# Kernel optimization log

Hardware: AMD Instinct MI355X
Metric: run time of the kernel (lower is better)

The kernel has to match this reference:

```python
import jax, jax.numpy as jnp
import numpy as np

D_MODEL = 2048
N_HEADS = 32
N_KV_HEADS = 8
HEAD_DIM = D_MODEL // N_HEADS  # 64
N_REP = N_HEADS // N_KV_HEADS  # 4
SCALE = HEAD_DIM ** -0.5


def _rope_tables(seq_len):
    inv_freq = 1.0 / (10000.0 ** (jnp.arange(0, HEAD_DIM, 2, dtype=jnp.float32) / HEAD_DIM))
    t = jnp.arange(seq_len, dtype=jnp.float32)
    freqs = jnp.outer(t, inv_freq)  # [S, HEAD_DIM/2]
    return jnp.cos(freqs), jnp.sin(freqs)


def _apply_rope(x, cos, sin):
    # x: [b, h, s, d]; interleaved even/odd rotation, matching torch stack+flatten
    x_r, x_i = x[..., ::2], x[..., 1::2]
    out_r = x_r * cos - x_i * sin
    out_i = x_r * sin + x_i * cos
    out = jnp.stack([out_r, out_i], axis=-1)  # [b,h,s,d/2,2]
    return out.reshape(x.shape)


def setup_inputs() -> dict:
    key = jax.random.key(0)
    ks = jax.random.split(key, 5)
    bs, seq_len = 2, 2048
    std = D_MODEL ** -0.5
    x = jax.random.normal(ks[0], (bs, seq_len, D_MODEL), dtype=jnp.float32)
    wq = jax.random.normal(ks[1], (N_HEADS * HEAD_DIM, D_MODEL), dtype=jnp.float32) * std
    wk = jax.random.normal(ks[2], (N_KV_HEADS * HEAD_DIM, D_MODEL), dtype=jnp.float32) * std
    wv = jax.random.normal(ks[3], (N_KV_HEADS * HEAD_DIM, D_MODEL), dtype=jnp.float32) * std
    wo = jax.random.normal(ks[4], (D_MODEL, N_HEADS * HEAD_DIM), dtype=jnp.float32) * std
    return {"x": x, "wq": wq, "wk": wk, "wv": wv, "wo": wo}


def reference(x, wq, wk, wv, wo):
    bs, seq_len, _ = x.shape
    # fused-style QKV projections (nn.Linear: x @ W.T)
    q = (x @ wq.T).reshape(bs, seq_len, N_HEADS, HEAD_DIM).transpose(0, 2, 1, 3)
    k = (x @ wk.T).reshape(bs, seq_len, N_KV_HEADS, HEAD_DIM).transpose(0, 2, 1, 3)
    v = (x @ wv.T).reshape(bs, seq_len, N_KV_HEADS, HEAD_DIM).transpose(0, 2, 1, 3)
    cos, sin = _rope_tables(seq_len)  # [S, HEAD_DIM/2], broadcast over b,h
    q = _apply_rope(q, cos, sin)
    k = _apply_rope(k, cos, sin)
    # GQA: repeat KV heads to match Q heads
    k = jnp.repeat(k, N_REP, axis=1)  # [b, H, s, d]
    v = jnp.repeat(v, N_REP, axis=1)
    attn = jnp.einsum('bhqd,bhkd->bhqk', q, k) * SCALE
    causal = jnp.triu(jnp.ones((seq_len, seq_len), dtype=bool), k=1)
    attn = jnp.where(causal, -jnp.inf, attn)
    attn = jax.nn.softmax(attn, axis=-1)
    out = jnp.einsum('bhqk,bhkd->bhqd', attn, v)
    out = out.transpose(0, 2, 1, 3).reshape(bs, seq_len, D_MODEL)
    return out @ wo.T
```

## Files before the change

kernel.cpp:

```cpp
#include <hip/hip_runtime.h>

#define SEQ    2048
#define DM     2048
#define QKVN   3072
#define VTR    64

typedef short s16x8 __attribute__((ext_vector_type(8)));
typedef float f32x4 __attribute__((ext_vector_type(4)));
typedef unsigned short us;

#define MFMA(a,b,c) __builtin_amdgcn_mfma_f32_16x16x32_bf16((a),(b),(c),0,0,0)

__device__ __forceinline__ float bf2f(us u) {
    unsigned v = ((unsigned)u) << 16;
    return __builtin_bit_cast(float, v);
}
__device__ __forceinline__ us f2bf(float f) {
    unsigned u = __builtin_bit_cast(unsigned, f);
    u += 0x7FFFu + ((u >> 16) & 1u);
    return (us)(u >> 16);
}
__device__ __forceinline__ void stp(us* p, float f) {
    *p = (us)(__builtin_bit_cast(unsigned, f) >> 16);
}
__device__ __forceinline__ void glds16(const us* g, us* l) {
    __builtin_amdgcn_global_load_lds((__attribute__((address_space(1))) void*)g,
                                     (__attribute__((address_space(3))) void*)l, 16, 0, 0);
}

__global__ __launch_bounds__(256) void cvt_all(const float* __restrict__ x,
                                               const float* __restrict__ wq,
                                               const float* __restrict__ wk,
                                               const float* __restrict__ wv,
                                               const float* __restrict__ wo,
                                               us* __restrict__ xb,
                                               us* __restrict__ wdst) {
    int i = blockIdx.x * blockDim.x + threadIdx.x;
    const float* src;
    int off;
    if (i < 2097152)      { src = x;  off = 0; }
    else {
        int j = i - 2097152;
        if (j < 1048576)      { src = wq; off = 2097152; }
        else if (j < 1310720) { src = wk; off = 2097152 + 1048576; }
        else if (j < 1572864) { src = wv; off = 2097152 + 1310720; }
        else                  { src = wo; off = 2097152 + 1572864; }
    }
    float4 v = ((const float4*)src)[i - off];
    ushort4 o;
    o.x = f2bf(v.x); o.y = f2bf(v.y); o.z = f2bf(v.z); o.w = f2bf(v.w);
    ((ushort4*)(i < 2097152 ? xb : wdst))[i < 2097152 ? i : i - 2097152] = o;
}

template <typename OutT, bool ROPE>
__global__ __launch_bounds__(256) void gemm_bt(const us* __restrict__ A, const us* __restrict__ W,
                                               OutT* __restrict__ C, int M, int N, int K) {
    __shared__ us la[128 * 32];
    __shared__ us lb[128 * 32];
    const int tid = threadIdx.x, lane = tid & 63, wave = tid >> 6;
    const int quad = lane >> 4, lr = lane & 15;
    const int m0 = blockIdx.x * 128, n0 = blockIdx.y * 128;
    const int wm = (wave & 1) * 64, wn = (wave >> 1) * 64;

    f32x4 acc[4][4] = {};

    const int r0 = wave * 32 + (lane >> 2);
    const int c0 = (lane & 3) * 8;
    const us* ga0 = A + (size_t)(m0 + r0) * K + c0;
    const us* ga1 = A + (size_t)(m0 + r0 + 16) * K + c0;
    const us* gb0 = W + (size_t)(n0 + r0) * K + c0;
    const us* gb1 = W + (size_t)(n0 + r0 + 16) * K + c0;
    us* lpa0 = &la[(wave * 32) * 32];
    us* lpa1 = &la[(wave * 32 + 16) * 32];
    us* lpb0 = &lb[(wave * 32) * 32];
    us* lpb1 = &lb[(wave * 32 + 16) * 32];

    for (int k0 = 0; k0 < K; k0 += 32) {
        glds16(ga0 + k0, lpa0);
        glds16(ga1 + k0, lpa1);
        glds16(gb0 + k0, lpb0);
        glds16(gb1 + k0, lpb1);
        __syncthreads();
        s16x8 af[4], bf[4];
#pragma unroll
        for (int i = 0; i < 4; i++) af[i] = *(const s16x8*)&la[(wm + i * 16 + lr) * 32 + quad * 8];
#pragma unroll
        for (int j = 0; j < 4; j++) bf[j] = *(const s16x8*)&lb[(wn + j * 16 + lr) * 32 + quad * 8];
#pragma unroll
        for (int i = 0; i < 4; i++)
#pragma unroll
            for (int j = 0; j < 4; j++)
                acc[i][j] = MFMA(af[i], bf[j], acc[i][j]);
        __syncthreads();
    }

#pragma unroll
    for (int i = 0; i < 4; i++)
#pragma unroll
        for (int j = 0; j < 4; j++)
#pragma unroll
            for (int r = 0; r < 4; r++) {
                int row = m0 + wm + i * 16 + quad * 4 + r;
                int col = n0 + wn + j * 16 + lr;
                float v = acc[i][j][r];
                if (ROPE && n0 < 2560) {
                    int pair = (col >> 1) & 31;
                    float inv = exp2f((float)pair * (-13.2877124f / 32.0f));
                    float ang = (float)(row & (SEQ - 1)) * inv;
                    float c = __cosf(ang), sn = __sinf(ang);
                    float p = __shfl_xor(v, 1);
                    v = v * c + ((col & 1) ? p * sn : -p * sn);
                }
                if constexpr (sizeof(OutT) == 2)
                    C[(size_t)row * N + col] = f2bf(v);
                else
                    C[(size_t)row * N + col] = v;
            }
}

__global__ __launch_bounds__(256) void transpose_v(const us* __restrict__ qkv, us* __restrict__ vt) {
    __shared__ us tile[64][72];
    const int s0 = blockIdx.x * 64;
    const int bk = blockIdx.y;
    const int b = bk >> 3, kvh = bk & 7;
    const int t = threadIdx.x;
    const int r = t >> 3, cg = (t & 7) * 8;
#pragma unroll
    for (int p = 0; p < 2; p++) {
        int rr = r + p * 32;
        *(s16x8*)&tile[rr][cg] =
            *(const s16x8*)(qkv + (size_t)(b * SEQ + s0 + rr) * QKVN + 2560 + kvh * 64 + cg);
    }
    __syncthreads();
#pragma unroll
    for (int p = 0; p < 2; p++) {
        int d = r + p * 32;
        s16x8 val;
#pragma unroll
        for (int u = 0; u < 8; u++) val[u] = tile[cg + u][d];
        *(s16x8*)(vt + ((size_t)bk * VTR + d) * SEQ + s0 + cg) = val;
    }
}

__global__ __launch_bounds__(256, 2) void flash_attn(const us* __restrict__ qkv,
                                                     const us* __restrict__ vt,
                                                     us* __restrict__ o) {
    __shared__ us P[4][4][16 * 72];
    const int bh = blockIdx.y, b = bh >> 5, h = bh & 31, kvh = h >> 2;
    const int wave = threadIdx.x >> 6, lane = threadIdx.x & 63;
    const int quad = lane >> 4, lr = lane & 15;
    const int p = ((int)blockIdx.x + (int)(blockIdx.y >> 3)) & 7;
    const int qts[4] = {p, 15 - p, 16 + p, 31 - p};
    const us* kbase = qkv + (size_t)b * SEQ * QKVN + 2048 + kvh * 64;
    const us* vb = vt + (size_t)(b * 8 + kvh) * VTR * SEQ;
    const float QS = 0.125f * 1.44269504f;

    s16x8 onesb;
    const short ov = (lr == 0) ? (short)0x3F80 : (short)0;
#pragma unroll
    for (int j = 0; j < 8; j++) onesb[j] = ov;

    int q0[4];
    s16x8 qa[4][2];
#pragma unroll
    for (int t = 0; t < 4; t++) {
        q0[t] = qts[t] * 64 + wave * 16;
        const us* qb = qkv + (size_t)(b * SEQ + q0[t]) * QKVN + h * 64;
        qa[t][0] = *(const s16x8*)(qb + (size_t)lr * QKVN + quad * 8);
        qa[t][1] = *(const s16x8*)(qb + (size_t)lr * QKVN + 32 + quad * 8);
#pragma unroll
        for (int j = 0; j < 8; j++) {
            qa[t][0][j] = (short)f2bf(bf2f((us)qa[t][0][j]) * QS);
            qa[t][1][j] = (short)f2bf(bf2f((us)qa[t][1][j]) * QS);
        }
    }

    f32x4 oacc[4][5] = {};
    s16x8 kf[8], vf[8];
    {
        const us* kp = kbase + (size_t)lr * QKVN;
#pragma unroll
        for (int nb = 0; nb < 4; nb++) {
            kf[2 * nb]     = *(const s16x8*)(kp + (size_t)nb * 16 * QKVN + quad * 8);
            kf[2 * nb + 1] = *(const s16x8*)(kp + (size_t)nb * 16 * QKVN + 32 + quad * 8);
        }
#pragma unroll
        for (int n = 0; n < 4; n++)
#pragma unroll
            for (int kc = 0; kc < 2; kc++)
                vf[n * 2 + kc] = *(const s16x8*)(vb + (size_t)(n * 16 + lr) * SEQ +
                                                 kc * 32 + quad * 8);
    }

    auto qk_tile = [&](int t, f32x4* sc) {
#pragma unroll
        for (int nb = 0; nb < 4; nb++) {
            sc[nb] = f32x4{0.f, 0.f, 0.f, 0.f};
            sc[nb] = MFMA(qa[t][0], kf[2 * nb], sc[nb]);
            sc[nb] = MFMA(qa[t][1], kf[2 * nb + 1], sc[nb]);
        }
    };
    auto store_tile = [&](int t, const f32x4* sc, int kb) {
        us* Pt = &P[wave][t][0];
        if (kb == qts[t]) {
#pragma unroll
            for (int nb = 0; nb < 4; nb++)
#pragma unroll
                for (int r = 0; r < 4; r++) {
                    int key = kb * 64 + nb * 16 + lr, row = q0[t] + quad * 4 + r;
                    float s = (key > row) ? -1e30f : sc[nb][r];
                    stp(&Pt[(quad * 4 + r) * 72 + nb * 16 + lr], exp2f(s));
                }
        } else {
#pragma unroll
            for (int nb = 0; nb < 4; nb++)
#pragma unroll
                for (int r = 0; r < 4; r++)
                    stp(&Pt[(quad * 4 + r) * 72 + nb * 16 + lr], exp2f(sc[nb][r]));
        }
    };

    const int kbmax = qts[3];
    for (int kb = 0; kb <= kbmax; kb++) {
        const bool a0 = (kb <= qts[0]), a1 = (kb <= qts[1]), a2 = (kb <= qts[2]);
        f32x4 sa[4], sb[4];
        if (a0) qk_tile(0, sa);
        if (a1) qk_tile(1, sb);
        if (a0) store_tile(0, sa, kb);
        if (a1) store_tile(1, sb, kb);
        if (a2) qk_tile(2, sa);
        qk_tile(3, sb);
        if (kb < kbmax) {
            const us* kp = kbase + (size_t)((kb + 1) * 64 + lr) * QKVN;
#pragma unroll
            for (int nb = 0; nb < 4; nb++) {
                kf[2 * nb]     = *(const s16x8*)(kp + (size_t)nb * 16 * QKVN + quad * 8);
                kf[2 * nb + 1] = *(const s16x8*)(kp + (size_t)nb * 16 * QKVN + 32 + quad * 8);
            }
        }
        if (a2) store_tile(2, sa, kb);
        store_tile(3, sb, kb);
        asm volatile("s_waitcnt lgkmcnt(0)" ::: "memory");
        __builtin_amdgcn_s_setprio(1);
#pragma unroll
        for (int t = 0; t < 4; t++) {
            if (kb <= qts[t]) {
#pragma unroll
                for (int kc = 0; kc < 2; kc++) {
                    s16x8 pa = *(const s16x8*)&P[wave][t][lr * 72 + kc * 32 + quad * 8];
#pragma unroll
                    for (int n = 0; n < 4; n++)
                        oacc[t][n] = MFMA(pa, vf[n * 2 + kc], oacc[t][n]);
                    oacc[t][4] = MFMA(pa, onesb, oacc[t][4]);
                }
            }
        }
        __builtin_amdgcn_s_setprio(0);
        if (kb < kbmax) {
#pragma unroll
            for (int n = 0; n < 4; n++)
#pragma unroll
                for (int kc = 0; kc < 2; kc++)
                    vf[n * 2 + kc] = *(const s16x8*)(vb + (size_t)(n * 16 + lr) * SEQ +
                                                     (kb + 1) * 64 + kc * 32 + quad * 8);
        }
    }

#pragma unroll
    for (int t = 0; t < 4; t++)
#pragma unroll
        for (int r = 0; r < 4; r++) {
            float l = __shfl(oacc[t][4][r], lane & 48);
            float li = 1.0f / l;
#pragma unroll
            for (int n = 0; n < 4; n++)
                o[(size_t)(b * SEQ + q0[t] + quad * 4 + r) * DM + h * 64 + n * 16 + lr] =
                    f2bf(oacc[t][n][r] * li);
        }
}

extern "C" void kernel_launch(void* const* d_in, const int* in_sizes, int n_in,
                              void* d_out, int out_size, void* d_ws, size_t ws_size,
                              hipStream_t stream) {
    const float* x  = (const float*)d_in[0];
    const float* wq = (const float*)d_in[1];
    const float* wk = (const float*)d_in[2];
    const float* wv = (const float*)d_in[3];
    const float* wo = (const float*)d_in[4];
    float* out = (float*)d_out;

    char* ws = (char*)d_ws;
    const size_t MB = 1024 * 1024;
    us* xb     = (us*)(ws + 0 * MB);
    us* abuf   = (us*)(ws + 0 * MB);
    us* wqkvb  = (us*)(ws + 16 * MB);
    us* wob    = (us*)(ws + 28 * MB);
    us* qkvbuf = (us*)(ws + 36 * MB);
    us* vtbuf  = (us*)(ws + 60 * MB);

    dim3 blk(256);
    cvt_all<<<dim3(18432), blk, 0, stream>>>(x, wq, wk, wv, wo, xb, wqkvb);

    gemm_bt<us, true><<<dim3(32, 24), blk, 0, stream>>>(xb, wqkvb, qkvbuf, 4096, 3072, 2048);
    transpose_v<<<dim3(32, 16), blk, 0, stream>>>(qkvbuf, vtbuf);
    flash_attn<<<dim3(8, 64), blk, 0, stream>>>(qkvbuf, vtbuf, abuf);
    gemm_bt<float, false><<<dim3(32, 16), blk, 0, stream>>>(abuf, wob, out, 4096, 2048, 2048);
}
```

Measured before the change: 384.1 us.

## Rewrite GEMM as 256x256 tiled, double-buffered, swizzled 8-wave pipelined kernel

Replaces the 128x128, 4-wave, single-buffered GEMM with a 256x256 tile per 512-thread block. It uses a K-step of 64, double-buffered LDS halves, XOR-swizzled LDS layout and interleaved quarter-tile loads overlapped with MFMA phases, plus s_setprio around the MFMA bursts. The goal is to hide global-load latency, raise arithmetic intensity per LDS byte and cut bank conflicts. The cost is 128KB of LDS per block and far fewer blocks (192 and 128), which lowers occupancy and may leave CUs idle on a 256-CU part.

```diff
diff --git a/kernel.cpp b/kernel.cpp
--- a/kernel.cpp
+++ b/kernel.cpp
@@ -53,55 +53,132 @@
 }
 
 template <typename OutT, bool ROPE>
-__global__ __launch_bounds__(256) void gemm_bt(const us* __restrict__ A, const us* __restrict__ W,
-                                               OutT* __restrict__ C, int M, int N, int K) {
-    __shared__ us la[128 * 32];
-    __shared__ us lb[128 * 32];
+__global__ __launch_bounds__(512) void gemm_bt2(const us* __restrict__ A, const us* __restrict__ W,
+                                                OutT* __restrict__ C, int M, int N, int K) {
+    __shared__ us lA[2][2][128 * 64];
+    __shared__ us lB[2][2][128 * 64];
     const int tid = threadIdx.x, lane = tid & 63, wave = tid >> 6;
     const int quad = lane >> 4, lr = lane & 15;
-    const int m0 = blockIdx.x * 128, n0 = blockIdx.y * 128;
-    const int wm = (wave & 1) * 64, wn = (wave >> 1) * 64;
-
-    f32x4 acc[4][4] = {};
-
-    const int r0 = wave * 32 + (lane >> 2);
-    const int c0 = (lane & 3) * 8;
-    const us* ga0 = A + (size_t)(m0 + r0) * K + c0;
-    const us* ga1 = A + (size_t)(m0 + r0 + 16) * K + c0;
-    const us* gb0 = W + (size_t)(n0 + r0) * K + c0;
-    const us* gb1 = W + (size_t)(n0 + r0 + 16) * K + c0;
-    us* lpa0 = &la[(wave * 32) * 32];
-    us* lpa1 = &la[(wave * 32 + 16) * 32];
-    us* lpb0 = &lb[(wave * 32) * 32];
-    us* lpb1 = &lb[(wave * 32 + 16) * 32];
-
-    for (int k0 = 0; k0 < K; k0 += 32) {
-        glds16(ga0 + k0, lpa0);
-        glds16(ga1 + k0, lpa1);
-        glds16(gb0 + k0, lpb0);
-        glds16(gb1 + k0, lpb1);
-        __syncthreads();
-        s16x8 af[4], bf[4];
-#pragma unroll
-        for (int i = 0; i < 4; i++) af[i] = *(const s16x8*)&la[(wm + i * 16 + lr) * 32 + quad * 8];
-#pragma unroll
-        for (int j = 0; j < 4; j++) bf[j] = *(const s16x8*)&lb[(wn + j * 16 + lr) * 32 + quad * 8];
+    const int mh = wave >> 2;
+    const int wnx = wave & 3;
+    const int bh = wnx >> 1, br0 = (wnx & 1) * 64;
+    const int m0 = blockIdx.x * 256, n0 = blockIdx.y * 256;
+
+    const int srow = tid >> 3;
+    const int scol = ((tid & 7) ^ (srow & 7)) * 8;
+    const int sdst = srow * 64 + (tid & 7) * 8;
+
+    const us* gA = A + (size_t)m0 * K;
+    const us* gB = W + (size_t)n0 * K;
+
+    auto stageH = [&](int s) {
+        const int t = s >> 2, ty = s & 3, par = t & 1;
+        const us* src;
+        us* dst;
+        if (ty < 2) { src = gA + (size_t)(ty * 128) * K;       dst = &lA[par][ty][0]; }
+        else        { src = gB + (size_t)((ty - 2) * 128) * K; dst = &lB[par][ty - 2][0]; }
+        src += t * 64;
+        glds16(src + (size_t)srow * K + scol,        dst + sdst);
+        glds16(src + (size_t)(srow + 64) * K + scol, dst + sdst + 64 * 64);
+    };
+
+    const int rsw = (lr & 7) << 3;
+    auto rdA = [&](int par, int kk, int i) {
+        return *(const s16x8*)&lA[par][mh][(i * 16 + lr) * 64 + ((kk * 32 + quad * 8) ^ rsw)];
+    };
+    auto rdB = [&](int par, int kk, int j) {
+        return *(const s16x8*)&lB[par][bh][(br0 + j * 16 + lr) * 64 + ((kk * 32 + quad * 8) ^ rsw)];
+    };
+
+    f32x4 acc[8][4] = {};
+    const int NT = K / 64;
+
+    stageH(0); stageH(1); stageH(2); stageH(3); stageH(4);
+    asm volatile("s_waitcnt vmcnt(2)" ::: "memory");
+    __builtin_amdgcn_s_barrier();
+
+    s16x8 af[2][4], ag[2][4], bfr[2][2], bg[2][2];
+    for (int t = 0; t < NT; ++t) {
+        const int par = t & 1;
+#pragma unroll
+        for (int kk = 0; kk < 2; kk++) {
+#pragma unroll
+            for (int i = 0; i < 4; i++) af[kk][i] = rdA(par, kk, i);
+#pragma unroll
+            for (int j = 0; j < 2; j++) bfr[kk][j] = rdB(par, kk, j);
+        }
+        if (t + 1 < NT) stageH(4 * (t + 1) + 1);
+        __builtin_amdgcn_s_barrier();
+        asm volatile("s_waitcnt lgkmcnt(0)" ::: "memory");
+        __builtin_amdgcn_s_setprio(1);
 #pragma unroll
         for (int i = 0; i < 4; i++)
 #pragma unroll
-            for (int j = 0; j < 4; j++)
-                acc[i][j] = MFMA(af[i], bf[j], acc[i][j]);
-        __syncthreads();
-    }
-
-#pragma unroll
-    for (int i = 0; i < 4; i++)
+            for (int j = 0; j < 2; j++)
+#pragma unroll
+                for (int kk = 0; kk < 2; kk++)
+                    acc[i][j] = MFMA(af[kk][i], bfr[kk][j], acc[i][j]);
+        __builtin_amdgcn_s_setprio(0);
+        __builtin_amdgcn_s_barrier();
+#pragma unroll
+        for (int kk = 0; kk < 2; kk++)
+#pragma unroll
+            for (int j = 0; j < 2; j++) bg[kk][j] = rdB(par, kk, 2 + j);
+        if (t + 1 < NT) stageH(4 * (t + 1) + 2);
+        __builtin_amdgcn_s_barrier();
+        asm volatile("s_waitcnt lgkmcnt(0)" ::: "memory");
+        __builtin_amdgcn_s_setprio(1);
+#pragma unroll
+        for (int i = 0; i < 4; i++)
+#pragma unroll
+            for (int j = 0; j < 2; j++)
+#pragma unroll
+                for (int kk = 0; kk < 2; kk++)
+                    acc[i][2 + j] = MFMA(af[kk][i], bg[kk][j], acc[i][2 + j]);
+        __builtin_amdgcn_s_setprio(0);
+        __builtin_amdgcn_s_barrier();
+#pragma unroll
+        for (int kk = 0; kk < 2; kk++)
+#pragma unroll
+            for (int i = 0; i < 4; i++) ag[kk][i] = rdA(par, kk, 4 + i);
+        if (t + 1 < NT) stageH(4 * (t + 1) + 3);
+        __builtin_amdgcn_s_barrier();
+        asm volatile("s_waitcnt lgkmcnt(0)" ::: "memory");
+        __builtin_amdgcn_s_setprio(1);
+#pragma unroll
+        for (int i = 0; i < 4; i++)
+#pragma unroll
+            for (int j = 0; j < 2; j++)
+#pragma unroll
+                for (int kk = 0; kk < 2; kk++)
+                    acc[4 + i][j] = MFMA(ag[kk][i], bfr[kk][j], acc[4 + i][j]);
+        __builtin_amdgcn_s_setprio(0);
+        __builtin_amdgcn_s_barrier();
+        if (t + 2 < NT) stageH(4 * (t + 2));
+        __builtin_amdgcn_s_setprio(1);
+#pragma unroll
+        for (int i = 0; i < 4; i++)
+#pragma unroll
+            for (int j = 0; j < 2; j++)
+#pragma unroll
+                for (int kk = 0; kk < 2; kk++)
+                    acc[4 + i][2 + j] = MFMA(ag[kk][i], bg[kk][j], acc[4 + i][2 + j]);
+        __builtin_amdgcn_s_setprio(0);
+        if (t + 1 < NT) {
+            if (t + 2 < NT) asm volatile("s_waitcnt vmcnt(2)" ::: "memory");
+            else            asm volatile("s_waitcnt vmcnt(0)" ::: "memory");
+            __builtin_amdgcn_s_barrier();
+        }
+    }
+
+#pragma unroll
+    for (int i = 0; i < 8; i++)
 #pragma unroll
         for (int j = 0; j < 4; j++)
 #pragma unroll
             for (int r = 0; r < 4; r++) {
-                int row = m0 + wm + i * 16 + quad * 4 + r;
-                int col = n0 + wn + j * 16 + lr;
+                int row = m0 + mh * 128 + i * 16 + quad * 4 + r;
+                int col = n0 + wnx * 64 + j * 16 + lr;
                 float v = acc[i][j][r];
                 if (ROPE && n0 < 2560) {
                     int pair = (col >> 1) & 31;
@@ -301,8 +378,8 @@
     dim3 blk(256);
     cvt_all<<<dim3(18432), blk, 0, stream>>>(x, wq, wk, wv, wo, xb, wqkvb);
 
-    gemm_bt<us, true><<<dim3(32, 24), blk, 0, stream>>>(xb, wqkvb, qkvbuf, 4096, 3072, 2048);
+    gemm_bt2<us, true><<<dim3(16, 12), dim3(512), 0, stream>>>(xb, wqkvb, qkvbuf, 4096, 3072, 2048);
     transpose_v<<<dim3(32, 16), blk, 0, stream>>>(qkvbuf, vtbuf);
     flash_attn<<<dim3(8, 64), blk, 0, stream>>>(qkvbuf, vtbuf, abuf);
-    gemm_bt<float, false><<<dim3(32, 16), blk, 0, stream>>>(abuf, wob, out, 4096, 2048, 2048);
-}
+    gemm_bt2<float, false><<<dim3(16, 8), dim3(512), 0, stream>>>(abuf, wob, out, 4096, 2048, 2048);
+}
```

Result: faster. 361.7 us (-5.8%).
